# Kernel tuning notes

Hardware: AMD Instinct MI355X
Metric: run time of the kernel (lower is better)

## Reference

```python
import jax, jax.numpy as jnp
import numpy as np

B, N, S, D = 2, 2048, 2048, 256
NHEAD = 4
HDIM = D // NHEAD
EPS = 1e-5


def embed_rotary(x, cos, sin):
    # x, cos, sin: [B,N,D]; rotate pairs (even, odd)
    x2 = jnp.stack([-x[..., 1::2], x[..., ::2]], axis=-1).reshape(x.shape)
    return x * cos + x2 * sin


def layernorm(x, g, b):
    mu = jnp.mean(x, axis=-1, keepdims=True)
    var = jnp.var(x, axis=-1, keepdims=True)
    return (x - mu) * jax.lax.rsqrt(var + EPS) * g + b


def setup_inputs() -> dict:
    key = jax.random.key(0)
    ks = jax.random.split(key, 10)
    w = 0.05
    return {
        "x": jax.random.normal(ks[0], (B, N, D), jnp.float32),
        "source": jax.random.normal(ks[1], (B, S, D), jnp.float32),
        "x_pe": jax.random.normal(ks[2], (B, N, D, 2), jnp.float32),
        "source_pe": jax.random.normal(ks[3], (B, S, D, 2), jnp.float32),
        "Wq": jax.random.normal(ks[4], (D, D), jnp.float32) * w,
        "Wk": jax.random.normal(ks[5], (D, D), jnp.float32) * w,
        "Wv": jax.random.normal(ks[6], (D, D), jnp.float32) * w,
        "Wm": jax.random.normal(ks[7], (D, D), jnp.float32) * w,
        "W1": jax.random.normal(ks[8], (2 * D, 2 * D), jnp.float32) * w,
        "W2": jax.random.normal(ks[9], (2 * D, D), jnp.float32) * w,
        "g1": jnp.ones((D,), jnp.float32),
        "b1": jnp.zeros((D,), jnp.float32),
        "g2": jnp.ones((D,), jnp.float32),
        "b2": jnp.zeros((D,), jnp.float32),
    }


def reference(x, source, x_pe, source_pe, Wq, Wk, Wv, Wm, W1, W2, g1, b1, g2, b2):
    bs = x.shape[0]
    # projections (no bias)
    qw = x @ Wq            # [B,N,D]
    kw = source @ Wk       # [B,S,D]
    vw = source @ Wv       # [B,S,D]
    # inline rotary PE applied before head split
    qw = embed_rotary(qw, x_pe[..., 0], x_pe[..., 1])
    kw = embed_rotary(kw, source_pe[..., 0], source_pe[..., 1])
    qw = qw.reshape(bs, -1, NHEAD, HDIM)
    kw = kw.reshape(bs, -1, NHEAD, HDIM)
    vw = vw.reshape(bs, -1, NHEAD, HDIM)
    # attention (no mask)
    a = jnp.einsum('nlhd,nshd->nlsh', qw, kw) / jnp.sqrt(jnp.float32(HDIM))
    a = jax.nn.softmax(a, axis=2)
    o = jnp.einsum('nlsh,nshd->nlhd', a, vw).reshape(bs, -1, NHEAD * HDIM)
    message = layernorm(o @ Wm, g1, b1)
    h = jax.nn.relu(jnp.concatenate([x, message], axis=2) @ W1)
    message = layernorm(h @ W2, g2, b2)
    return x + message
```

## Files before the change

kernel.cpp:

```cpp
#include <hip/hip_runtime.h>
#include <hip/hip_bf16.h>

#define NN 2048
#define DD 256
#define HD 64
#define LN_EPS 1e-5f
#define SPLIT 4
#define CHUNK (NN / SPLIT)
#define KVB 64

typedef __bf16 bf16x8 __attribute__((ext_vector_type(8)));
typedef __bf16 bf16x4 __attribute__((ext_vector_type(4)));
typedef float  f32x4  __attribute__((ext_vector_type(4)));

static __device__ __forceinline__ bf16x8 make8(bf16x4 lo, bf16x4 hi) {
    return bf16x8{lo[0],lo[1],lo[2],lo[3],hi[0],hi[1],hi[2],hi[3]};
}
static __device__ __forceinline__ bf16x8 ldfrag(const __bf16* p) {
    bf16x4 lo = *(const bf16x4*)p;
    bf16x4 hi = *(const bf16x4*)(p + 16);
    return make8(lo, hi);
}

__global__ void wtall_kernel(const float* __restrict__ Wq, const float* __restrict__ Wk,
                             const float* __restrict__ Wv, const float* __restrict__ Wm,
                             const float* __restrict__ W1, const float* __restrict__ W2,
                             __bf16* __restrict__ Wqt, __bf16* __restrict__ Wkvt,
                             __bf16* __restrict__ Wmt, __bf16* __restrict__ W1t,
                             __bf16* __restrict__ W2t)
{
    int i = blockIdx.x * 256 + threadIdx.x;
    if (i < 65536) {
        int n = i >> 8, k = i & 255;
        Wqt[i] = (__bf16)Wq[k * 256 + n];
    } else if (i < 196608) {
        int j = i - 65536;
        int n = j >> 8, k = j & 255;
        Wkvt[j] = (__bf16)(n < 256 ? Wk[k * 256 + n] : Wv[k * 256 + n - 256]);
    } else if (i < 262144) {
        int j = i - 196608;
        int n = j >> 8, k = j & 255;
        Wmt[j] = (__bf16)Wm[k * 256 + n];
    } else if (i < 524288) {
        int j = i - 262144;
        int n = j >> 9, k = j & 511;
        W1t[j] = (__bf16)W1[k * 512 + n];
    } else if (i < 655360) {
        int j = i - 524288;
        int n = j >> 9, k = j & 511;
        W2t[j] = (__bf16)W2[k * 256 + n];
    }
}

template<int EPI, bool ABF>
__global__ __launch_bounds__(256) void gemm_kernel(
    const void* __restrict__ Av, const __bf16* __restrict__ Bt,
    void* __restrict__ Cv, void* __restrict__ Cv2, const float* __restrict__ pe,
    int M, int N, int K)
{
    __shared__ alignas(16) __bf16 As[64][72];
    __shared__ alignas(16) __bf16 Bs[64][72];

    const int t = threadIdx.x;
    const int rowbase = blockIdx.y * 64;
    const int colbase = blockIdx.x * 64;
    const int w = t >> 6, lane = t & 63;
    const int wr = w >> 1, wc = w & 1;
    const int lr = lane & 15, lg = lane >> 4;

    const int sr = t >> 2;
    const int scc = (t & 3) * 16;

    f32x4 acc[2][2] = {};

    for (int kb = 0; kb < K; kb += 64) {
        __syncthreads();
        {
            long grow = rowbase + sr;
            if (ABF) {
                const __bf16* A = (const __bf16*)Av;
                bf16x8 a0 = *(const bf16x8*)&A[grow * K + kb + scc];
                bf16x8 a1 = *(const bf16x8*)&A[grow * K + kb + scc + 8];
                *(bf16x8*)&As[sr][scc]     = a0;
                *(bf16x8*)&As[sr][scc + 8] = a1;
            } else {
                const float* A = (const float*)Av;
                const float4* p = (const float4*)&A[grow * K + kb + scc];
                float4 a0 = p[0], a1 = p[1], a2 = p[2], a3 = p[3];
                *(bf16x8*)&As[sr][scc] = bf16x8{
                    (__bf16)a0.x,(__bf16)a0.y,(__bf16)a0.z,(__bf16)a0.w,
                    (__bf16)a1.x,(__bf16)a1.y,(__bf16)a1.z,(__bf16)a1.w};
                *(bf16x8*)&As[sr][scc + 8] = bf16x8{
                    (__bf16)a2.x,(__bf16)a2.y,(__bf16)a2.z,(__bf16)a2.w,
                    (__bf16)a3.x,(__bf16)a3.y,(__bf16)a3.z,(__bf16)a3.w};
            }
        }
        {
            long gn = colbase + sr;
            bf16x8 b0 = *(const bf16x8*)&Bt[gn * K + kb + scc];
            bf16x8 b1 = *(const bf16x8*)&Bt[gn * K + kb + scc + 8];
            *(bf16x8*)&Bs[sr][scc]     = b0;
            *(bf16x8*)&Bs[sr][scc + 8] = b1;
        }
        __syncthreads();

        #pragma unroll
        for (int kk = 0; kk < 2; ++kk) {
            bf16x8 af[2], bfr[2];
            #pragma unroll
            for (int mt = 0; mt < 2; ++mt)
                af[mt] = ldfrag(&As[wr*32 + mt*16 + lr][kk*32 + 4*lg]);
            #pragma unroll
            for (int nt = 0; nt < 2; ++nt)
                bfr[nt] = ldfrag(&Bs[wc*32 + nt*16 + lr][kk*32 + 4*lg]);
            #pragma unroll
            for (int mt = 0; mt < 2; ++mt)
                #pragma unroll
                for (int nt = 0; nt < 2; ++nt)
                    acc[mt][nt] = __builtin_amdgcn_mfma_f32_16x16x32_bf16(af[mt], bfr[nt], acc[mt][nt], 0, 0, 0);
        }
    }

    #pragma unroll
    for (int mt = 0; mt < 2; ++mt) {
        #pragma unroll
        for (int nt = 0; nt < 2; ++nt) {
            #pragma unroll
            for (int r = 0; r < 4; ++r) {
                long grow = rowbase + wr*32 + mt*16 + lg*4 + r;
                int  gcol = colbase + wc*32 + nt*16 + lr;
                float val = acc[mt][nt][r];
                if (EPI == 1) {
                    float partner = __shfl_xor(val, 1);
                    const float* pp = &pe[(grow * DD + gcol) * 2];
                    float c = pp[0], s = pp[1];
                    val = (gcol & 1) ? (val * c + partner * s) : (val * c - partner * s);
                    ((__bf16*)Cv)[grow * N + gcol] = (__bf16)val;
                } else if (EPI == 2) {
                    ((float*)Cv)[grow * N + gcol] = val;
                } else if (EPI == 3) {
                    ((__bf16*)Cv)[grow * N + gcol] = (__bf16)fmaxf(val, 0.f);
                } else {
                    if (gcol < 256) {
                        float partner = __shfl_xor(val, 1);
                        const float* pp = &pe[(grow * DD + gcol) * 2];
                        float c = pp[0], s = pp[1];
                        val = (gcol & 1) ? (val * c + partner * s) : (val * c - partner * s);
                        ((__bf16*)Cv)[grow * DD + gcol] = (__bf16)val;
                    } else {
                        ((__bf16*)Cv2)[grow * DD + gcol - 256] = (__bf16)val;
                    }
                }
            }
        }
    }
}

__global__ __launch_bounds__(256) void attn_part_kernel(
    const __bf16* __restrict__ q, const __bf16* __restrict__ kk,
    const __bf16* __restrict__ v, float* __restrict__ op, float* __restrict__ ml)
{
    __shared__ alignas(16) __bf16 Qs[64][72];
    __shared__ alignas(16) __bf16 Ks[64][72];
    __shared__ alignas(16) __bf16 Vt[64][72];
    __shared__ alignas(16) __bf16 Ps[4][16][72];

    const int t = threadIdx.x;
    const int qb = blockIdx.x * 64;
    const int h  = blockIdx.y;
    const int z  = blockIdx.z;
    const int b  = z >> 2, sp = z & 3;
    const int w = t >> 6, lane = t & 63;
    const int lr = lane & 15, lg = lane >> 4;
    const long row0 = (long)b * NN;

    #pragma unroll
    for (int i = 0; i < 2; ++i) {
        int idx = t + i * 256;
        int r = idx >> 3, cc = (idx & 7) * 8;
        *(bf16x8*)&Qs[r][cc] = *(const bf16x8*)&q[(row0 + qb + r) * DD + h * HD + cc];
    }
    __syncthreads();
    bf16x8 qf[2];
    qf[0] = ldfrag(&Qs[w*16 + lr][4*lg]);
    qf[1] = ldfrag(&Qs[w*16 + lr][32 + 4*lg]);

    f32x4 acco[4] = {};
    float mrun[4], lrun[4];
    #pragma unroll
    for (int r = 0; r < 4; ++r) { mrun[r] = -INFINITY; lrun[r] = 0.f; }

    const int sr = t >> 2, scc = (t & 3) * 16;
    for (int sb = sp * CHUNK; sb < sp * CHUNK + CHUNK; sb += KVB) {
        __syncthreads();
        {
            const __bf16* kp = &kk[(row0 + sb + sr) * DD + h * HD + scc];
            *(bf16x8*)&Ks[sr][scc]     = *(const bf16x8*)kp;
            *(bf16x8*)&Ks[sr][scc + 8] = *(const bf16x8*)(kp + 8);
            const __bf16* vp = &v[(row0 + sb + sr) * DD + h * HD + scc];
            bf16x8 v0 = *(const bf16x8*)vp;
            bf16x8 v1 = *(const bf16x8*)(vp + 8);
            #pragma unroll
            for (int j = 0; j < 8; ++j) {
                int hd = scc + j;
                Vt[hd][sr ^ (4 * ((hd >> 3) & 7))] = v0[j];
                int hd2 = scc + 8 + j;
                Vt[hd2][sr ^ (4 * ((hd2 >> 3) & 7))] = v1[j];
            }
        }
        __syncthreads();

        f32x4 accs[4] = {};
        #pragma unroll
        for (int nt = 0; nt < 4; ++nt)
            #pragma unroll
            for (int ks = 0; ks < 2; ++ks) {
                bf16x8 kf = ldfrag(&Ks[nt*16 + lr][ks*32 + 4*lg]);
                accs[nt] = __builtin_amdgcn_mfma_f32_16x16x32_bf16(qf[ks], kf, accs[nt], 0, 0, 0);
            }

        float sc[4];
        #pragma unroll
        for (int r = 0; r < 4; ++r) {
            float s0 = accs[0][r] * 0.125f, s1 = accs[1][r] * 0.125f;
            float s2 = accs[2][r] * 0.125f, s3 = accs[3][r] * 0.125f;
            float mx = fmaxf(fmaxf(s0, s1), fmaxf(s2, s3));
            #pragma unroll
            for (int m = 1; m < 16; m <<= 1) mx = fmaxf(mx, __shfl_xor(mx, m));
            float mnew = fmaxf(mrun[r], mx);
            float p0 = __expf(s0 - mnew), p1 = __expf(s1 - mnew);
            float p2 = __expf(s2 - mnew), p3 = __expf(s3 - mnew);
            float rs = (p0 + p1) + (p2 + p3);
            #pragma unroll
            for (int m = 1; m < 16; m <<= 1) rs += __shfl_xor(rs, m);
            sc[r] = __expf(mrun[r] - mnew);
            lrun[r] = lrun[r] * sc[r] + rs;
            mrun[r] = mnew;
            Ps[w][lg*4 + r][lr]      = (__bf16)p0;
            Ps[w][lg*4 + r][lr + 16] = (__bf16)p1;
            Ps[w][lg*4 + r][lr + 32] = (__bf16)p2;
            Ps[w][lg*4 + r][lr + 48] = (__bf16)p3;
        }
        asm volatile("s_waitcnt lgkmcnt(0)" ::: "memory");
        __builtin_amdgcn_sched_barrier(0);

        bf16x8 pf[2];
        pf[0] = ldfrag(&Ps[w][lr][4*lg]);
        pf[1] = ldfrag(&Ps[w][lr][32 + 4*lg]);

        #pragma unroll
        for (int nt = 0; nt < 4; ++nt) {
            #pragma unroll
            for (int r = 0; r < 4; ++r) acco[nt][r] *= sc[r];
            int d = nt*16 + lr;
            int xsw = 4 * ((d >> 3) & 7);
            const __bf16* vrow = &Vt[d][0];
            #pragma unroll
            for (int ks = 0; ks < 2; ++ks) {
                bf16x4 lo = *(const bf16x4*)&vrow[(ks*32 + 4*lg) ^ xsw];
                bf16x4 hi = *(const bf16x4*)&vrow[(ks*32 + 16 + 4*lg) ^ xsw];
                acco[nt] = __builtin_amdgcn_mfma_f32_16x16x32_bf16(pf[ks], make8(lo, hi), acco[nt], 0, 0, 0);
            }
        }
    }

    long pr = (long)(sp * 2 + b) * 2048 + qb + w*16 + lg*4;
    #pragma unroll
    for (int nt = 0; nt < 4; ++nt)
        #pragma unroll
        for (int r = 0; r < 4; ++r)
            op[(pr + r) * 256 + h * HD + nt*16 + lr] = acco[nt][r];
    if (lr == 0) {
        #pragma unroll
        for (int r = 0; r < 4; ++r) {
            long mi = ((long)(sp * 2 + b) * 4 + h) * 2048 + (qb + w*16 + lg*4 + r);
            *(float2*)&ml[mi * 2] = make_float2(mrun[r], lrun[r]);
        }
    }
}

__global__ __launch_bounds__(256) void attn_comb_kernel(
    const float* __restrict__ op, const float* __restrict__ ml, __bf16* __restrict__ o)
{
    int row = blockIdx.x;
    int t = threadIdx.x;
    int b = row >> 11, n = row & 2047;
    int h = t >> 6;
    float m[SPLIT], l[SPLIT];
    #pragma unroll
    for (int sp = 0; sp < SPLIT; ++sp) {
        float2 v2 = *(const float2*)&ml[(((long)(sp*2 + b) * 4 + h) * 2048 + n) * 2];
        m[sp] = v2.x; l[sp] = v2.y;
    }
    float M = fmaxf(fmaxf(m[0], m[1]), fmaxf(m[2], m[3]));
    float L = 0.f, oa = 0.f;
    #pragma unroll
    for (int sp = 0; sp < SPLIT; ++sp) {
        float wgt = __expf(m[sp] - M);
        L  += l[sp] * wgt;
        oa += op[((long)(sp*2 + b) * 2048 + n) * 256 + t] * wgt;
    }
    o[(long)row * 256 + t] = (__bf16)(oa / L);
}

__global__ __launch_bounds__(256) void ln1_cat_kernel(
    const float* __restrict__ m1, const float* __restrict__ x,
    const float* __restrict__ g, const float* __restrict__ bb,
    __bf16* __restrict__ cat)
{
    __shared__ float red[2][4];
    int row = blockIdx.x, t = threadIdx.x;
    float val = m1[(long)row * DD + t];
    float s = val, sq = val * val;
    #pragma unroll
    for (int m = 1; m < 64; m <<= 1) { s += __shfl_xor(s, m); sq += __shfl_xor(sq, m); }
    int w = t >> 6;
    if ((t & 63) == 0) { red[0][w] = s; red[1][w] = sq; }
    __syncthreads();
    s  = red[0][0] + red[0][1] + red[0][2] + red[0][3];
    sq = red[1][0] + red[1][1] + red[1][2] + red[1][3];
    float mean = s * (1.f / DD);
    float var  = sq * (1.f / DD) - mean * mean;
    float y = (val - mean) * rsqrtf(var + LN_EPS) * g[t] + bb[t];
    cat[(long)row * 512 + 256 + t] = (__bf16)y;
    cat[(long)row * 512 + t]       = (__bf16)x[(long)row * DD + t];
}

__global__ __launch_bounds__(256) void ln2_res_kernel(
    const float* __restrict__ m2, const float* __restrict__ x,
    const float* __restrict__ g, const float* __restrict__ bb,
    float* __restrict__ out)
{
    __shared__ float red[2][4];
    int row = blockIdx.x, t = threadIdx.x;
    float val = m2[(long)row * DD + t];
    float s = val, sq = val * val;
    #pragma unroll
    for (int m = 1; m < 64; m <<= 1) { s += __shfl_xor(s, m); sq += __shfl_xor(sq, m); }
    int w = t >> 6;
    if ((t & 63) == 0) { red[0][w] = s; red[1][w] = sq; }
    __syncthreads();
    s  = red[0][0] + red[0][1] + red[0][2] + red[0][3];
    sq = red[1][0] + red[1][1] + red[1][2] + red[1][3];
    float mean = s * (1.f / DD);
    float var  = sq * (1.f / DD) - mean * mean;
    float y = (val - mean) * rsqrtf(var + LN_EPS) * g[t] + bb[t];
    out[(long)row * DD + t] = x[(long)row * DD + t] + y;
}

extern "C" void kernel_launch(void* const* d_in, const int* in_sizes, int n_in,
                              void* d_out, int out_size, void* d_ws, size_t ws_size,
                              hipStream_t stream)
{
    const float* x   = (const float*)d_in[0];
    const float* src = (const float*)d_in[1];
    const float* xpe = (const float*)d_in[2];
    const float* spe = (const float*)d_in[3];
    const float* Wq  = (const float*)d_in[4];
    const float* Wk  = (const float*)d_in[5];
    const float* Wv  = (const float*)d_in[6];
    const float* Wm  = (const float*)d_in[7];
    const float* W1  = (const float*)d_in[8];
    const float* W2  = (const float*)d_in[9];
    const float* g1  = (const float*)d_in[10];
    const float* b1  = (const float*)d_in[11];
    const float* g2  = (const float*)d_in[12];
    const float* b2  = (const float*)d_in[13];

    char* ws = (char*)d_ws;
    size_t off = 0;
    auto alloc = [&](size_t bytes) -> void* {
        void* p = ws + off; off += (bytes + 255) & ~(size_t)255; return p;
    };
    __bf16* Wqt  = (__bf16*)alloc(256 * 256 * 2);
    __bf16* Wkvt = (__bf16*)alloc(512 * 256 * 2);
    __bf16* Wmt  = (__bf16*)alloc(256 * 256 * 2);
    __bf16* W1t  = (__bf16*)alloc(512 * 512 * 2);
    __bf16* W2t  = (__bf16*)alloc(256 * 512 * 2);
    __bf16* qws  = (__bf16*)alloc((size_t)4096 * 256 * 2);
    __bf16* kws  = (__bf16*)alloc((size_t)4096 * 256 * 2);
    __bf16* vws  = (__bf16*)alloc((size_t)4096 * 256 * 2);
    __bf16* ows  = (__bf16*)alloc((size_t)4096 * 256 * 2);
    char*   big  = (char*)alloc((size_t)16 * 1024 * 1024);
    float*  op   = (float*)big;
    float*  m1   = (float*)big;
    __bf16* cat  = (__bf16*)(big + (size_t)4  * 1024 * 1024);
    __bf16* hws  = (__bf16*)(big + (size_t)8  * 1024 * 1024);
    float*  m2   = (float*)(big + (size_t)12 * 1024 * 1024);
    float*  ml   = (float*)alloc((size_t)SPLIT * 2 * 4 * 2048 * 2 * 4);

    wtall_kernel<<<2560, 256, 0, stream>>>(Wq, Wk, Wv, Wm, W1, W2,
                                           Wqt, Wkvt, Wmt, W1t, W2t);

    gemm_kernel<1, false><<<dim3(4, 64), 256, 0, stream>>>(x,   Wqt,  qws, nullptr, xpe, 4096, 256, 256);
    gemm_kernel<4, false><<<dim3(8, 64), 256, 0, stream>>>(src, Wkvt, kws, vws,     spe, 4096, 512, 256);

    attn_part_kernel<<<dim3(32, 4, 2 * SPLIT), 256, 0, stream>>>(qws, kws, vws, op, ml);
    attn_comb_kernel<<<4096, 256, 0, stream>>>(op, ml, ows);

    gemm_kernel<2, true><<<dim3(4, 64), 256, 0, stream>>>(ows, Wmt, m1, nullptr, nullptr, 4096, 256, 256);
    ln1_cat_kernel<<<4096, 256, 0, stream>>>(m1, x, g1, b1, cat);
    gemm_kernel<3, true><<<dim3(8, 64), 256, 0, stream>>>(cat, W1t, hws, nullptr, nullptr, 4096, 512, 512);
    gemm_kernel<2, true><<<dim3(4, 64), 256, 0, stream>>>(hws, W2t, m2, nullptr, nullptr, 4096, 256, 512);
    ln2_res_kernel<<<4096, 256, 0, stream>>>(m2, x, g2, b2, (float*)d_out);
}
```

Baseline: 192.4 us.

## Stage GEMM and attention tiles via direct global-to-LDS loads with XOR swizzle

Replaces register-staged tile copies in the GEMMs and in the attention Q/K loads with global_load_lds direct-to-LDS transfers into an unpadded, XOR-swizzled layout, and reads fragments back through a matching swizzle. x and source are now converted to bf16 inside the weight-prep kernel so all GEMMs read bf16. The Q and KV projections are merged into one launch. This cuts VGPR traffic and launch count, at the cost of an extra pass over the inputs and dependence on the swizzle matching the LDS write pattern.

```diff
diff --git a/kernel.cpp b/kernel.cpp
--- a/kernel.cpp
+++ b/kernel.cpp
@@ -22,12 +22,36 @@
     return make8(lo, hi);
 }
 
+static __device__ __forceinline__ void stage64(const __bf16* __restrict__ g, int ldg,
+                                               __bf16* lds, int t) {
+    const int w = t >> 6, lane = t & 63;
+    #pragma unroll
+    for (int i = 0; i < 2; ++i) {
+        int chunk = (w + 4*i) * 64 + lane;
+        int r = chunk >> 3;
+        int j = (chunk & 7) ^ (r & 7);
+        __builtin_amdgcn_global_load_lds(
+            (const __attribute__((address_space(1))) void*)(g + (long)r * ldg + j * 8),
+            (__attribute__((address_space(3))) void*)(lds + (w + 4*i) * 512),
+            16, 0, 0);
+    }
+}
+static __device__ __forceinline__ bf16x8 ldfrag_swz(const __bf16* lds, int row, int cbyte) {
+    const char* p = (const char*)(lds + row * 64);
+    int sw = (row & 7) << 4;
+    bf16x4 lo = *(const bf16x4*)(p + (cbyte ^ sw));
+    bf16x4 hi = *(const bf16x4*)(p + ((cbyte + 32) ^ sw));
+    return make8(lo, hi);
+}
+
 __global__ void wtall_kernel(const float* __restrict__ Wq, const float* __restrict__ Wk,
                              const float* __restrict__ Wv, const float* __restrict__ Wm,
                              const float* __restrict__ W1, const float* __restrict__ W2,
+                             const float* __restrict__ x,  const float* __restrict__ src,
                              __bf16* __restrict__ Wqt, __bf16* __restrict__ Wkvt,
                              __bf16* __restrict__ Wmt, __bf16* __restrict__ W1t,
-                             __bf16* __restrict__ W2t)
+                             __bf16* __restrict__ W2t, __bf16* __restrict__ xb,
+                             __bf16* __restrict__ srcb)
 {
     int i = blockIdx.x * 256 + threadIdx.x;
     if (i < 65536) {
@@ -49,59 +73,56 @@
         int j = i - 524288;
         int n = j >> 9, k = j & 511;
         W2t[j] = (__bf16)W2[k * 256 + n];
-    }
-}
-
-template<int EPI, bool ABF>
-__global__ __launch_bounds__(256) void gemm_kernel(
-    const void* __restrict__ Av, const __bf16* __restrict__ Bt,
-    void* __restrict__ Cv, void* __restrict__ Cv2, const float* __restrict__ pe,
+    } else if (i < 786432) {
+        int j = i - 655360;
+        const float4* p = (const float4*)&x[(long)j * 8];
+        float4 a0 = p[0], a1 = p[1];
+        *(bf16x8*)&xb[(long)j * 8] = bf16x8{
+            (__bf16)a0.x,(__bf16)a0.y,(__bf16)a0.z,(__bf16)a0.w,
+            (__bf16)a1.x,(__bf16)a1.y,(__bf16)a1.z,(__bf16)a1.w};
+    } else if (i < 917504) {
+        int j = i - 786432;
+        const float4* p = (const float4*)&src[(long)j * 8];
+        float4 a0 = p[0], a1 = p[1];
+        *(bf16x8*)&srcb[(long)j * 8] = bf16x8{
+            (__bf16)a0.x,(__bf16)a0.y,(__bf16)a0.z,(__bf16)a0.w,
+            (__bf16)a1.x,(__bf16)a1.y,(__bf16)a1.z,(__bf16)a1.w};
+    }
+}
+
+template<int EPI>
+__global__ __launch_bounds__(256) void gemm2_kernel(
+    const __bf16* __restrict__ A1, const __bf16* __restrict__ A2,
+    const __bf16* __restrict__ B1, const __bf16* __restrict__ B2,
+    void* __restrict__ C1, void* __restrict__ C2, void* __restrict__ C3,
+    const float* __restrict__ pe1, const float* __restrict__ pe2,
     int M, int N, int K)
 {
-    __shared__ alignas(16) __bf16 As[64][72];
-    __shared__ alignas(16) __bf16 Bs[64][72];
+    __shared__ alignas(16) __bf16 As[64 * 64];
+    __shared__ alignas(16) __bf16 Bs[64 * 64];
 
     const int t = threadIdx.x;
     const int rowbase = blockIdx.y * 64;
-    const int colbase = blockIdx.x * 64;
     const int w = t >> 6, lane = t & 63;
     const int wr = w >> 1, wc = w & 1;
     const int lr = lane & 15, lg = lane >> 4;
 
-    const int sr = t >> 2;
-    const int scc = (t & 3) * 16;
+    const __bf16* Ap = A1;
+    const __bf16* Bp = B1;
+    const float*  pe = pe1;
+    int colbase = blockIdx.x * 64;
+    bool isQ = true;
+    if (EPI == 5) {
+        isQ = blockIdx.x < 4;
+        if (!isQ) { Ap = A2; Bp = B2; pe = pe2; colbase = (blockIdx.x - 4) * 64; }
+    }
 
     f32x4 acc[2][2] = {};
 
     for (int kb = 0; kb < K; kb += 64) {
         __syncthreads();
-        {
-            long grow = rowbase + sr;
-            if (ABF) {
-                const __bf16* A = (const __bf16*)Av;
-                bf16x8 a0 = *(const bf16x8*)&A[grow * K + kb + scc];
-                bf16x8 a1 = *(const bf16x8*)&A[grow * K + kb + scc + 8];
-                *(bf16x8*)&As[sr][scc]     = a0;
-                *(bf16x8*)&As[sr][scc + 8] = a1;
-            } else {
-                const float* A = (const float*)Av;
-                const float4* p = (const float4*)&A[grow * K + kb + scc];
-                float4 a0 = p[0], a1 = p[1], a2 = p[2], a3 = p[3];
-                *(bf16x8*)&As[sr][scc] = bf16x8{
-                    (__bf16)a0.x,(__bf16)a0.y,(__bf16)a0.z,(__bf16)a0.w,
-                    (__bf16)a1.x,(__bf16)a1.y,(__bf16)a1.z,(__bf16)a1.w};
-                *(bf16x8*)&As[sr][scc + 8] = bf16x8{
-                    (__bf16)a2.x,(__bf16)a2.y,(__bf16)a2.z,(__bf16)a2.w,
-                    (__bf16)a3.x,(__bf16)a3.y,(__bf16)a3.z,(__bf16)a3.w};
-            }
-        }
-        {
-            long gn = colbase + sr;
-            bf16x8 b0 = *(const bf16x8*)&Bt[gn * K + kb + scc];
-            bf16x8 b1 = *(const bf16x8*)&Bt[gn * K + kb + scc + 8];
-            *(bf16x8*)&Bs[sr][scc]     = b0;
-            *(bf16x8*)&Bs[sr][scc + 8] = b1;
-        }
+        stage64(Ap + (long)rowbase * K + kb, K, As, t);
+        stage64(Bp + (long)colbase * K + kb, K, Bs, t);
         __syncthreads();
 
         #pragma unroll
@@ -109,10 +130,10 @@
             bf16x8 af[2], bfr[2];
             #pragma unroll
             for (int mt = 0; mt < 2; ++mt)
-                af[mt] = ldfrag(&As[wr*32 + mt*16 + lr][kk*32 + 4*lg]);
+                af[mt] = ldfrag_swz(As, wr*32 + mt*16 + lr, kk*64 + lg*8);
             #pragma unroll
             for (int nt = 0; nt < 2; ++nt)
-                bfr[nt] = ldfrag(&Bs[wc*32 + nt*16 + lr][kk*32 + 4*lg]);
+                bfr[nt] = ldfrag_swz(Bs, wc*32 + nt*16 + lr, kk*64 + lg*8);
             #pragma unroll
             for (int mt = 0; mt < 2; ++mt)
                 #pragma unroll
@@ -130,25 +151,19 @@
                 long grow = rowbase + wr*32 + mt*16 + lg*4 + r;
                 int  gcol = colbase + wc*32 + nt*16 + lr;
                 float val = acc[mt][nt][r];
-                if (EPI == 1) {
-                    float partner = __shfl_xor(val, 1);
-                    const float* pp = &pe[(grow * DD + gcol) * 2];
-                    float c = pp[0], s = pp[1];
-                    val = (gcol & 1) ? (val * c + partner * s) : (val * c - partner * s);
-                    ((__bf16*)Cv)[grow * N + gcol] = (__bf16)val;
-                } else if (EPI == 2) {
-                    ((float*)Cv)[grow * N + gcol] = val;
+                if (EPI == 2) {
+                    ((float*)C1)[grow * N + gcol] = val;
                 } else if (EPI == 3) {
-                    ((__bf16*)Cv)[grow * N + gcol] = (__bf16)fmaxf(val, 0.f);
+                    ((__bf16*)C1)[grow * N + gcol] = (__bf16)fmaxf(val, 0.f);
                 } else {
-                    if (gcol < 256) {
+                    if (isQ || gcol < 256) {
                         float partner = __shfl_xor(val, 1);
                         const float* pp = &pe[(grow * DD + gcol) * 2];
                         float c = pp[0], s = pp[1];
                         val = (gcol & 1) ? (val * c + partner * s) : (val * c - partner * s);
-                        ((__bf16*)Cv)[grow * DD + gcol] = (__bf16)val;
+                        ((__bf16*)(isQ ? C1 : C2))[grow * DD + gcol] = (__bf16)val;
                     } else {
-                        ((__bf16*)Cv2)[grow * DD + gcol - 256] = (__bf16)val;
+                        ((__bf16*)C3)[grow * DD + gcol - 256] = (__bf16)val;
                     }
                 }
             }
@@ -160,8 +175,8 @@
     const __bf16* __restrict__ q, const __bf16* __restrict__ kk,
     const __bf16* __restrict__ v, float* __restrict__ op, float* __restrict__ ml)
 {
-    __shared__ alignas(16) __bf16 Qs[64][72];
-    __shared__ alignas(16) __bf16 Ks[64][72];
+    __shared__ alignas(16) __bf16 Qs[64 * 64];
+    __shared__ alignas(16) __bf16 Ks[64 * 64];
     __shared__ alignas(16) __bf16 Vt[64][72];
     __shared__ alignas(16) __bf16 Ps[4][16][72];
 
@@ -174,16 +189,11 @@
     const int lr = lane & 15, lg = lane >> 4;
     const long row0 = (long)b * NN;
 
-    #pragma unroll
-    for (int i = 0; i < 2; ++i) {
-        int idx = t + i * 256;
-        int r = idx >> 3, cc = (idx & 7) * 8;
-        *(bf16x8*)&Qs[r][cc] = *(const bf16x8*)&q[(row0 + qb + r) * DD + h * HD + cc];
-    }
+    stage64(q + (row0 + qb) * DD + h * HD, DD, Qs, t);
     __syncthreads();
     bf16x8 qf[2];
-    qf[0] = ldfrag(&Qs[w*16 + lr][4*lg]);
-    qf[1] = ldfrag(&Qs[w*16 + lr][32 + 4*lg]);
+    qf[0] = ldfrag_swz(Qs, w*16 + lr, lg*8);
+    qf[1] = ldfrag_swz(Qs, w*16 + lr, 64 + lg*8);
 
     f32x4 acco[4] = {};
     float mrun[4], lrun[4];
@@ -193,10 +203,8 @@
     const int sr = t >> 2, scc = (t & 3) * 16;
     for (int sb = sp * CHUNK; sb < sp * CHUNK + CHUNK; sb += KVB) {
         __syncthreads();
+        stage64(kk + (row0 + sb) * DD + h * HD, DD, Ks, t);
         {
-            const __bf16* kp = &kk[(row0 + sb + sr) * DD + h * HD + scc];
-            *(bf16x8*)&Ks[sr][scc]     = *(const bf16x8*)kp;
-            *(bf16x8*)&Ks[sr][scc + 8] = *(const bf16x8*)(kp + 8);
             const __bf16* vp = &v[(row0 + sb + sr) * DD + h * HD + scc];
             bf16x8 v0 = *(const bf16x8*)vp;
             bf16x8 v1 = *(const bf16x8*)(vp + 8);
@@ -215,7 +223,7 @@
         for (int nt = 0; nt < 4; ++nt)
             #pragma unroll
             for (int ks = 0; ks < 2; ++ks) {
-                bf16x8 kf = ldfrag(&Ks[nt*16 + lr][ks*32 + 4*lg]);
+                bf16x8 kf = ldfrag_swz(Ks, nt*16 + lr, ks*64 + lg*8);
                 accs[nt] = __builtin_amdgcn_mfma_f32_16x16x32_bf16(qf[ks], kf, accs[nt], 0, 0, 0);
             }
 
@@ -377,6 +385,8 @@
     __bf16* Wmt  = (__bf16*)alloc(256 * 256 * 2);
     __bf16* W1t  = (__bf16*)alloc(512 * 512 * 2);
     __bf16* W2t  = (__bf16*)alloc(256 * 512 * 2);
+    __bf16* xb   = (__bf16*)alloc((size_t)4096 * 256 * 2);
+    __bf16* srcb = (__bf16*)alloc((size_t)4096 * 256 * 2);
     __bf16* qws  = (__bf16*)alloc((size_t)4096 * 256 * 2);
     __bf16* kws  = (__bf16*)alloc((size_t)4096 * 256 * 2);
     __bf16* vws  = (__bf16*)alloc((size_t)4096 * 256 * 2);
@@ -389,18 +399,21 @@
     float*  m2   = (float*)(big + (size_t)12 * 1024 * 1024);
     float*  ml   = (float*)alloc((size_t)SPLIT * 2 * 4 * 2048 * 2 * 4);
 
-    wtall_kernel<<<2560, 256, 0, stream>>>(Wq, Wk, Wv, Wm, W1, W2,
-                                           Wqt, Wkvt, Wmt, W1t, W2t);
-
-    gemm_kernel<1, false><<<dim3(4, 64), 256, 0, stream>>>(x,   Wqt,  qws, nullptr, xpe, 4096, 256, 256);
-    gemm_kernel<4, false><<<dim3(8, 64), 256, 0, stream>>>(src, Wkvt, kws, vws,     spe, 4096, 512, 256);
+    wtall_kernel<<<3584, 256, 0, stream>>>(Wq, Wk, Wv, Wm, W1, W2, x, src,
+                                           Wqt, Wkvt, Wmt, W1t, W2t, xb, srcb);
+
+    gemm2_kernel<5><<<dim3(12, 64), 256, 0, stream>>>(
+        xb, srcb, Wqt, Wkvt, qws, kws, vws, xpe, spe, 4096, 256, 256);
 
     attn_part_kernel<<<dim3(32, 4, 2 * SPLIT), 256, 0, stream>>>(qws, kws, vws, op, ml);
     attn_comb_kernel<<<4096, 256, 0, stream>>>(op, ml, ows);
 
-    gemm_kernel<2, true><<<dim3(4, 64), 256, 0, stream>>>(ows, Wmt, m1, nullptr, nullptr, 4096, 256, 256);
+    gemm2_kernel<2><<<dim3(4, 64), 256, 0, stream>>>(
+        ows, nullptr, Wmt, nullptr, m1, nullptr, nullptr, nullptr, nullptr, 4096, 256, 256);
     ln1_cat_kernel<<<4096, 256, 0, stream>>>(m1, x, g1, b1, cat);
-    gemm_kernel<3, true><<<dim3(8, 64), 256, 0, stream>>>(cat, W1t, hws, nullptr, nullptr, 4096, 512, 512);
-    gemm_kernel<2, true><<<dim3(4, 64), 256, 0, stream>>>(hws, W2t, m2, nullptr, nullptr, 4096, 256, 512);
+    gemm2_kernel<3><<<dim3(8, 64), 256, 0, stream>>>(
+        cat, nullptr, W1t, nullptr, hws, nullptr, nullptr, nullptr, nullptr, 4096, 512, 512);
+    gemm2_kernel<2><<<dim3(4, 64), 256, 0, stream>>>(
+        hws, nullptr, W2t, nullptr, m2, nullptr, nullptr, nullptr, nullptr, 4096, 256, 512);
     ln2_res_kernel<<<4096, 256, 0, stream>>>(m2, x, g2, b2, (float*)d_out);
 }
```

New measurement: 187.6 us. 2.5% less time.
